# Kernel tuning notes

Hardware: AMD Instinct MI355X
Metric: run time of the kernel (lower is better)

The kernel has to match this reference:

```python
import jax, jax.numpy as jnp
import numpy as np

B, C, H = 2, 256, 64
INTER = 64


def setup_inputs() -> dict:
    key = jax.random.key(0)
    ks = jax.random.split(key, 10)
    scale = 1.0 / np.sqrt(C)
    x = jax.random.normal(ks[0], (B, C, H, H), dtype=jnp.float32)
    # binary hole mask (1 = foreground/hole region)
    mask = jnp.round(jax.random.uniform(ks[1], (B, 1, H, H), dtype=jnp.float32))
    def w(k, shape, s):
        return jax.random.normal(k, shape, dtype=jnp.float32) * s
    return {
        "x": x,
        "mask": mask,
        "w_theta_s": w(ks[2], (INTER, C), scale),
        "w_phi_s": w(ks[3], (INTER, C), scale),
        "w_gate_s": w(ks[4], (INTER, C), scale),
        "w_theta_c": w(ks[5], (INTER, C), scale),
        "w_phi_c": w(ks[6], (INTER, C), scale),
        "w_gate_c": w(ks[7], (INTER, C), scale),
        "w_out": w(ks[8], (C, INTER), 1.0 / np.sqrt(INTER)),
    }


def _nonlocal_branch(q_src, kv_src, w_theta, w_phi, w_gate):
    # q_src, kv_src: [B, C, N]; weights: [inter, C]
    K = jnp.einsum('oc,bcn->bon', w_theta, kv_src)   # [B, inter, N]
    Q = jnp.einsum('oc,bcn->bon', w_phi, q_src)      # [B, inter, N]
    score = jnp.einsum('bom,bon->bmn', Q, K)         # [B, Nq, Nk]
    score = jax.nn.softmax(score, axis=-1)
    V = jnp.einsum('oc,bcn->bon', w_gate, kv_src)    # [B, inter, N]
    feat = jnp.einsum('bon,bmn->bom', V, score)      # [B, inter, Nq]
    return feat, score


def reference(x, mask, w_theta_s, w_phi_s, w_gate_s,
              w_theta_c, w_phi_c, w_gate_c, w_out):
    b, c, h = x.shape[0], x.shape[1], x.shape[2]
    n = h * h
    fg = (x * mask).reshape(b, c, n)          # foreground tokens
    bg = (x * (1.0 - mask)).reshape(b, c, n)  # background tokens
    feat_self, score_self = _nonlocal_branch(fg, fg, w_theta_s, w_phi_s, w_gate_s)
    feat_cross, score_cross = _nonlocal_branch(fg, bg, w_theta_c, w_phi_c, w_gate_c)
    fused = jnp.einsum('co,bon->bcn', w_out, feat_self + feat_cross)
    feat = x + fused.reshape(b, c, h, h)
    return feat, score_self, score_cross
```

## Files before the change

kernel.cpp:

```cpp
#include <hip/hip_runtime.h>
#include <hip/hip_bf16.h>
#include <stdint.h>

#define NBATCH 2
#define NCH    256
#define NTOK   4096
#define NINT   64
#define CHW    64
#define QCOLS  1024
#define NCHQ   (QCOLS/CHW)

typedef float  f32x4  __attribute__((ext_vector_type(4)));
typedef __bf16 bf16x8 __attribute__((ext_vector_type(8)));
union U16x8 { uint4 u; bf16x8 b; };
union PK8   { uint4 u; unsigned short s[8]; };

#define SZBF      ((size_t)NTOK*NINT)
#define RL_OFF_B  ((size_t)4194304)

#define OUT_SELF  ((size_t)2097152)
#define OUT_CROSS ((size_t)35651584)
#define FPART_OFF_F (OUT_SELF)
#define LPART_OFF_F (OUT_SELF + (size_t)4194304)


__device__ inline unsigned short f2bf(float x){
  unsigned int u = __builtin_bit_cast(unsigned int, x);
  u = (u + 0x7FFFu + ((u>>16)&1u)) >> 16;
  return (unsigned short)u;
}
__device__ inline float bf2f(unsigned short s){
  unsigned int u = ((unsigned int)s)<<16;
  return __builtin_bit_cast(float, u);
}

__global__ __launch_bounds__(256) void k_proj(
    const float* __restrict__ x, const float* __restrict__ mask,
    const float* __restrict__ wts, const float* __restrict__ wps,
    const float* __restrict__ wgs, const float* __restrict__ wtc,
    const float* __restrict__ wpc, const float* __restrict__ wgc,
    char* __restrict__ ws)
{
  int nt = blockIdx.x;
  int j  = blockIdx.y;
  int b  = blockIdx.z;
  const float* W; int isBg, mode, arrH, arrL;
  switch (j) {
    case 0: W=wts; isBg=0; mode=2; arrH=2; arrL=3; break;
    case 1: W=wps; isBg=0; mode=0; arrH=0; arrL=1; break;
    case 2: W=wgs; isBg=0; mode=1; arrH=8; arrL=8; break;
    case 3: W=wpc; isBg=0; mode=0; arrH=4; arrL=5; break;
    case 4: W=wtc; isBg=1; mode=2; arrH=6; arrL=7; break;
    default:W=wgc; isBg=1; mode=1; arrH=9; arrL=9; break;
  }
  __shared__ float xm[128*64];
  __shared__ float msk[64];
  int t = threadIdx.x;
  if (t < 64) {
    float m = mask[(size_t)b*NTOK + nt*64 + t];
    msk[t] = isBg ? (1.0f - m) : m;
  }
  __syncthreads();
  const float* xb = x + (size_t)b*NCH*NTOK + nt*64;
  int nl = t & 63;
  int o0 = __builtin_amdgcn_readfirstlane((t>>6)*16);
  const float* Wr = W + (size_t)o0*256;
  float acc[16];
  #pragma unroll
  for (int i=0;i<16;i++) acc[i]=0.0f;
  for (int p=0; p<2; ++p){
    const float* xbp = xb + (size_t)p*128*NTOK;
    for (int it = 0; it < 32; ++it) {
      int flat = it*256 + t; int c = flat>>6, n2 = flat&63;
      xm[flat] = xbp[(size_t)c*NTOK + n2] * msk[n2];
    }
    __syncthreads();
    #pragma unroll 4
    for (int cc=0;cc<128;cc++){
      int c = p*128 + cc;
      float xv = xm[cc*64+nl];
      #pragma unroll
      for (int i=0;i<16;i++) acc[i] += Wr[i*256 + c] * xv;
    }
    __syncthreads();
  }
  int n = nt*64 + nl;
  if (mode==0){
    unsigned short* Ah = (unsigned short*)ws + ((size_t)b*10 + arrH)*SZBF;
    unsigned short* Al = (unsigned short*)ws + ((size_t)b*10 + arrL)*SZBF;
    #pragma unroll
    for (int i=0;i<16;i++){
      float v = acc[i];
      unsigned short h = f2bf(v);
      float r = v - bf2f(h);
      Ah[(size_t)n*NINT + o0+i] = h;
      Al[(size_t)n*NINT + o0+i] = f2bf(r);
    }
  } else if (mode==2){
    unsigned short* Ah = (unsigned short*)ws + ((size_t)b*10 + arrH)*SZBF;
    unsigned short* Al = (unsigned short*)ws + ((size_t)b*10 + arrL)*SZBF;
    int kk  = o0>>5;
    int q40 = (o0>>3)&3;
    size_t base = ((size_t)(n>>4)*2 + kk)*512 + (size_t)(q40*16 + (n&15))*8;
    #pragma unroll
    for (int run=0; run<2; ++run){
      PK8 ph, pl;
      #pragma unroll
      for (int i2=0;i2<8;i2++){
        float v = acc[run*8 + i2];
        unsigned short h = f2bf(v);
        ph.s[i2] = h;
        pl.s[i2] = f2bf(v - bf2f(h));
      }
      *(uint4*)(Ah + base + run*128) = ph.u;
      *(uint4*)(Al + base + run*128) = pl.u;
    }
  } else {
    unsigned short* VF = (unsigned short*)ws + ((size_t)b*10 + arrH)*SZBF;
    size_t cBase = (((size_t)nt*8 + ((nl>>5)&1)*4 + (o0>>4)))*512
                 + (size_t)((nl>>3)&3)*128 + (nl&7);
    #pragma unroll
    for (int i=0;i<16;i++) VF[cBase + (size_t)i*8] = f2bf(acc[i]);
  }
}

__global__ __launch_bounds__(256,2) void k_s1(char* __restrict__ ws, float* __restrict__ out)
{
  __shared__ __align__(16) unsigned short lP[4][1024];

  int blk = blockIdx.x;
  int xcd = blk & 7, idx = blk >> 3;
  int bbr = xcd >> 1;
  int unit = ((xcd & 1) << 6) | idx;
  int qtr = unit & 3, mb2 = unit >> 2;
  int b = bbr >> 1, br = bbr & 1;
  const unsigned short* Qh  = (const unsigned short*)ws + ((size_t)b*10 + (br?4:0))*SZBF;
  const unsigned short* Ql  = Qh + SZBF;
  const unsigned short* KFh = (const unsigned short*)ws + ((size_t)b*10 + (br?6:2))*SZBF;
  const unsigned short* KFl = KFh + SZBF;
  const unsigned short* VF  = (const unsigned short*)ws + ((size_t)b*10 + (br?9:8))*SZBF;

  int t = threadIdx.x, lane = t&63, w = t>>6;
  int rowb = lane&15, q4 = lane>>4, ko = q4*8;
  int mA = mb2*128 + w*16, mB = mA + 64;

  unsigned short* lPw = lP[w];

  U16x8 qhA[2], qlA[2], qhB[2], qlB[2];
  #pragma unroll
  for (int kk=0;kk<2;kk++){
    qhA[kk].u = *(const uint4*)(Qh + (size_t)(mA+rowb)*NINT + kk*32 + ko);
    qlA[kk].u = *(const uint4*)(Ql + (size_t)(mA+rowb)*NINT + kk*32 + ko);
    qhB[kk].u = *(const uint4*)(Qh + (size_t)(mB+rowb)*NINT + kk*32 + ko);
    qlB[kk].u = *(const uint4*)(Ql + (size_t)(mB+rowb)*NINT + kk*32 + ko);
  }

  f32x4 facA[4], facB[4];
  #pragma unroll
  for (int ot=0;ot<4;ot++){ facA[ot]=(f32x4){0,0,0,0}; facB[ot]=(f32x4){0,0,0,0}; }
  float LaccA = 0.0f, LaccB = 0.0f;

  for (int ch=0; ch<NCHQ; ++ch){
    int n0  = qtr*QCOLS + ch*CHW;
    int r16 = n0>>4;
    U16x8 akh[4][2], akl[4][2];
    #pragma unroll
    for (int t8=0; t8<4; ++t8)
      #pragma unroll
      for (int kk=0; kk<2; ++kk){
        size_t cb = ((size_t)(r16 + t8)*2 + kk)*512 + (size_t)lane*8;
        akh[t8][kk].u = *(const uint4*)(KFh + cb);
        akl[t8][kk].u = *(const uint4*)(KFl + cb);
      }
    U16x8 av[2][4];
    #pragma unroll
    for (int kk4=0; kk4<2; ++kk4)
      #pragma unroll
      for (int ot=0; ot<4; ++ot){
        size_t cb = ((size_t)(n0>>6)*8 + kk4*4 + ot)*512 + (size_t)lane*8;
        av[kk4][ot].u = *(const uint4*)(VF + cb);
      }

    #pragma unroll
    for (int hf=0; hf<2; ++hf){
      const U16x8* qh = hf ? qhB : qhA;
      const U16x8* ql = hf ? qlB : qlA;
      f32x4* fac      = hf ? facB : facA;
      float& Lacc     = hf ? LaccB : LaccA;
      #pragma unroll
      for (int t8=0; t8<4; ++t8){
        f32x4 s = {0.0f,0.0f,0.0f,0.0f};
        #pragma unroll
        for (int kk=0; kk<2; ++kk){
          s = __builtin_amdgcn_mfma_f32_16x16x32_bf16(akh[t8][kk].b, qh[kk].b, s, 0,0,0);
          s = __builtin_amdgcn_mfma_f32_16x16x32_bf16(akh[t8][kk].b, ql[kk].b, s, 0,0,0);
          s = __builtin_amdgcn_mfma_f32_16x16x32_bf16(akl[t8][kk].b, qh[kk].b, s, 0,0,0);
        }
        float p0=__expf(s[0]), p1=__expf(s[1]), p2=__expf(s[2]), p3=__expf(s[3]);
        Lacc += (p0+p1)+(p2+p3);
        unsigned int lo = (unsigned int)f2bf(p0) | ((unsigned int)f2bf(p1)<<16);
        unsigned int hi = (unsigned int)f2bf(p2) | ((unsigned int)f2bf(p3)<<16);
        uint2 pk; pk.x = lo; pk.y = hi;
        int g  = t8*2 + (q4>>1);
        int gs = g ^ (rowb&7);
        *(uint2*)(lPw + rowb*64 + gs*8 + (q4&1)*4) = pk;
      }
      #pragma unroll
      for (int kk4=0; kk4<2; ++kk4){
        int rs = (kk4*4 + q4) ^ (rowb&7);
        U16x8 pa;
        pa.u = *(const uint4*)(lPw + rowb*64 + rs*8);
        #pragma unroll
        for (int ot=0; ot<4; ++ot)
          fac[ot] = __builtin_amdgcn_mfma_f32_16x16x32_bf16(pa.b, av[kk4][ot].b, fac[ot], 0,0,0);
      }
    }
  }

  #pragma unroll
  for (int hf=0; hf<2; ++hf){
    int   m0   = hf ? mB : mA;
    float Lacc = hf ? LaccB : LaccA;
    f32x4* fac = hf ? facB : facA;
    #pragma unroll
    for (int d=16; d<64; d<<=1) Lacc += __shfl_xor(Lacc, d, 64);
    if (q4==0)
      out[LPART_OFF_F + (size_t)(bbr*4+qtr)*NTOK + m0 + rowb] = Lacc;
    float* FP = out + FPART_OFF_F + (size_t)(bbr*4+qtr)*NTOK*NINT;
    #pragma unroll
    for (int ot=0; ot<4; ++ot)
      #pragma unroll
      for (int r=0; r<4; ++r)
        FP[(size_t)(m0 + q4*4 + r)*NINT + ot*16 + rowb] = fac[ot][r];
  }
}

__global__ __launch_bounds__(256) void k_epi(
    const float* __restrict__ x, const float* __restrict__ wout,
    char* __restrict__ ws, float* __restrict__ out)
{
  int nt = blockIdx.x, b = blockIdx.y;
  int t = threadIdx.x;
  const float* FP = out + FPART_OFF_F;
  const float* LP = out + LPART_OFF_F;
  float* rL = (float*)(ws + RL_OFF_B);
  __shared__ float fs[32][65];
  __shared__ float rls[2][32];
  int b0 = b*2, b1 = b*2+1;
  if (t < 64){
    int hb = t>>5, rloc = t&31;
    int bb = b*2 + hb;
    int row = nt*32 + rloc;
    float L = 0.0f;
    #pragma unroll
    for (int q=0;q<4;q++) L += LP[(size_t)(bb*4+q)*NTOK + row];
    float r = 1.0f / L;
    rls[hb][rloc] = r;
    rL[(size_t)bb*NTOK + row] = r;
  }
  __syncthreads();
  for (int it=0; it<8; ++it){
    int flat = it*256 + t; int n_l = flat>>6, o = flat&63;
    int row = nt*32 + n_l;
    float s0=0.0f, s1=0.0f;
    #pragma unroll
    for (int q=0;q<4;q++){
      s0 += FP[((size_t)(b0*4+q)*NTOK + row)*NINT + o];
      s1 += FP[((size_t)(b1*4+q)*NTOK + row)*NINT + o];
    }
    fs[n_l][o] = s0*rls[0][n_l] + s1*rls[1][n_l];
  }
  __syncthreads();
  int nl = t&31, cg = t>>5, c0 = cg*32;
  float f[64];
  #pragma unroll
  for (int o=0;o<64;o++) f[o] = fs[nl][o];
  const float* wr = wout + (size_t)c0*64;
  int row = nt*32 + nl;
  for (int cc=0; cc<32; ++cc){
    int c = c0 + cc;
    float acc = x[((size_t)b*NCH + c)*NTOK + row];
    #pragma unroll
    for (int o=0;o<64;o++) acc += wr[cc*64+o]*f[o];
    out[((size_t)b*NCH + c)*NTOK + row] = acc;
  }
}

__global__ __launch_bounds__(256,4) void k_s2(const char* __restrict__ ws, float* __restrict__ out)
{
  int blk = blockIdx.x;
  int xcd = blk & 7, idx = blk >> 3;
  int bbr = xcd >> 1;
  int unit = ((xcd & 1) << 7) | idx;
  int qtr = unit & 3, mb = unit >> 2;
  int b = bbr >> 1, br = bbr & 1;
  const unsigned short* Qh  = (const unsigned short*)ws + ((size_t)b*10 + (br?4:0))*SZBF;
  const unsigned short* Ql  = Qh + SZBF;
  const unsigned short* KFh = (const unsigned short*)ws + ((size_t)b*10 + (br?6:2))*SZBF;
  const unsigned short* KFl = KFh + SZBF;

  int t = threadIdx.x, lane = t&63, w = t>>6;
  int rowb = lane&15, q4 = lane>>4, ko = q4*8;
  int m0 = mb*64 + w*16, mrow = m0 + rowb;

  float rLp = ((const float*)(ws + RL_OFF_B))[(size_t)bbr*NTOK + mrow];

  U16x8 qh[2], ql[2];
  #pragma unroll
  for (int kk=0;kk<2;kk++){
    qh[kk].u = *(const uint4*)(Qh + (size_t)mrow*NINT + kk*32 + ko);
    ql[kk].u = *(const uint4*)(Ql + (size_t)mrow*NINT + kk*32 + ko);
  }

  float* outS = out + (br ? OUT_CROSS : OUT_SELF) + (size_t)b*NTOK*NTOK;

  for (int ch=0; ch<NCHQ; ++ch){
    int n0  = qtr*QCOLS + ch*CHW;
    int r16 = n0>>4;
    #pragma unroll
    for (int t8=0; t8<4; ++t8){
      f32x4 s = {0.0f,0.0f,0.0f,0.0f};
      #pragma unroll
      for (int kk=0; kk<2; ++kk){
        size_t cb = ((size_t)(r16 + t8)*2 + kk)*512 + (size_t)lane*8;
        U16x8 ah, al;
        ah.u = *(const uint4*)(KFh + cb);
        al.u = *(const uint4*)(KFl + cb);
        s = __builtin_amdgcn_mfma_f32_16x16x32_bf16(ah.b, qh[kk].b, s, 0,0,0);
        s = __builtin_amdgcn_mfma_f32_16x16x32_bf16(ah.b, ql[kk].b, s, 0,0,0);
        s = __builtin_amdgcn_mfma_f32_16x16x32_bf16(al.b, qh[kk].b, s, 0,0,0);
      }
      f32x4 p;
      p[0] = __expf(s[0])*rLp; p[1] = __expf(s[1])*rLp;
      p[2] = __expf(s[2])*rLp; p[3] = __expf(s[3])*rLp;
      __builtin_nontemporal_store(p,
          (f32x4*)(outS + (size_t)mrow*NTOK + n0 + t8*16 + q4*4));
    }
  }
}

extern "C" void kernel_launch(void* const* d_in, const int* in_sizes, int n_in,
                              void* d_out, int out_size, void* d_ws, size_t ws_size,
                              hipStream_t stream)
{
  const float* x    = (const float*)d_in[0];
  const float* mask = (const float*)d_in[1];
  const float* wts  = (const float*)d_in[2];
  const float* wps  = (const float*)d_in[3];
  const float* wgs  = (const float*)d_in[4];
  const float* wtc  = (const float*)d_in[5];
  const float* wpc  = (const float*)d_in[6];
  const float* wgc  = (const float*)d_in[7];
  const float* wout = (const float*)d_in[8];
  float* out = (float*)d_out;
  char*  ws  = (char*)d_ws;
  (void)in_sizes; (void)n_in; (void)out_size; (void)ws_size;

  k_proj <<<dim3(64,6,NBATCH), 256, 0, stream>>>(x, mask, wts, wps, wgs, wtc, wpc, wgc, ws);
  k_s1   <<<dim3(512), 256, 0, stream>>>(ws, out);
  k_epi  <<<dim3(128,NBATCH), 256, 0, stream>>>(x, wout, ws, out);
  k_s2   <<<dim3(1024), 256, 0, stream>>>(ws, out);
}
```

Before: 487.0 us.

## Process two query row tiles per wave in k_s2, nontemporal partial stores

k_s2 now computes two 16-row query tiles per wave (128 rows per block), so each key fragment load from global memory feeds twice as many MFMAs. The grid is halved and launch bounds lowered to allow more registers. Separately, k_s1's partial feature and L stores and k_epi's partial loads use nontemporal hints to reduce cache pollution. The trade-off is fewer resident waves and higher register pressure in the store-bound score kernel.

```diff
diff --git a/kernel.cpp b/kernel.cpp
--- a/kernel.cpp
+++ b/kernel.cpp
@@ -225,13 +225,15 @@
     #pragma unroll
     for (int d=16; d<64; d<<=1) Lacc += __shfl_xor(Lacc, d, 64);
     if (q4==0)
-      out[LPART_OFF_F + (size_t)(bbr*4+qtr)*NTOK + m0 + rowb] = Lacc;
+      __builtin_nontemporal_store(Lacc,
+          out + LPART_OFF_F + (size_t)(bbr*4+qtr)*NTOK + m0 + rowb);
     float* FP = out + FPART_OFF_F + (size_t)(bbr*4+qtr)*NTOK*NINT;
     #pragma unroll
     for (int ot=0; ot<4; ++ot)
       #pragma unroll
       for (int r=0; r<4; ++r)
-        FP[(size_t)(m0 + q4*4 + r)*NINT + ot*16 + rowb] = fac[ot][r];
+        __builtin_nontemporal_store(fac[ot][r],
+            FP + (size_t)(m0 + q4*4 + r)*NINT + ot*16 + rowb);
   }
 }
 
@@ -265,8 +267,8 @@
     float s0=0.0f, s1=0.0f;
     #pragma unroll
     for (int q=0;q<4;q++){
-      s0 += FP[((size_t)(b0*4+q)*NTOK + row)*NINT + o];
-      s1 += FP[((size_t)(b1*4+q)*NTOK + row)*NINT + o];
+      s0 += __builtin_nontemporal_load(FP + ((size_t)(b0*4+q)*NTOK + row)*NINT + o);
+      s1 += __builtin_nontemporal_load(FP + ((size_t)(b1*4+q)*NTOK + row)*NINT + o);
     }
     fs[n_l][o] = s0*rls[0][n_l] + s1*rls[1][n_l];
   }
@@ -286,13 +288,13 @@
   }
 }
 
-__global__ __launch_bounds__(256,4) void k_s2(const char* __restrict__ ws, float* __restrict__ out)
+__global__ __launch_bounds__(256,2) void k_s2(const char* __restrict__ ws, float* __restrict__ out)
 {
   int blk = blockIdx.x;
   int xcd = blk & 7, idx = blk >> 3;
   int bbr = xcd >> 1;
-  int unit = ((xcd & 1) << 7) | idx;
-  int qtr = unit & 3, mb = unit >> 2;
+  int unit = ((xcd & 1) << 6) | idx;
+  int qtr = unit & 3, mb2 = unit >> 2;
   int b = bbr >> 1, br = bbr & 1;
   const unsigned short* Qh  = (const unsigned short*)ws + ((size_t)b*10 + (br?4:0))*SZBF;
   const unsigned short* Ql  = Qh + SZBF;
@@ -301,40 +303,55 @@
 
   int t = threadIdx.x, lane = t&63, w = t>>6;
   int rowb = lane&15, q4 = lane>>4, ko = q4*8;
-  int m0 = mb*64 + w*16, mrow = m0 + rowb;
-
-  float rLp = ((const float*)(ws + RL_OFF_B))[(size_t)bbr*NTOK + mrow];
-
-  U16x8 qh[2], ql[2];
+  int mA = mb2*128 + w*16, mB = mA + 64;
+  int mrowA = mA + rowb,   mrowB = mB + rowb;
+
+  const float* rL = (const float*)(ws + RL_OFF_B) + (size_t)bbr*NTOK;
+  float rLpA = rL[mrowA], rLpB = rL[mrowB];
+
+  U16x8 qhA[2], qlA[2], qhB[2], qlB[2];
   #pragma unroll
   for (int kk=0;kk<2;kk++){
-    qh[kk].u = *(const uint4*)(Qh + (size_t)mrow*NINT + kk*32 + ko);
-    ql[kk].u = *(const uint4*)(Ql + (size_t)mrow*NINT + kk*32 + ko);
+    qhA[kk].u = *(const uint4*)(Qh + (size_t)mrowA*NINT + kk*32 + ko);
+    qlA[kk].u = *(const uint4*)(Ql + (size_t)mrowA*NINT + kk*32 + ko);
+    qhB[kk].u = *(const uint4*)(Qh + (size_t)mrowB*NINT + kk*32 + ko);
+    qlB[kk].u = *(const uint4*)(Ql + (size_t)mrowB*NINT + kk*32 + ko);
   }
 
   float* outS = out + (br ? OUT_CROSS : OUT_SELF) + (size_t)b*NTOK*NTOK;
+  float* outA = outS + (size_t)mrowA*NTOK;
+  float* outB = outS + (size_t)mrowB*NTOK;
 
   for (int ch=0; ch<NCHQ; ++ch){
     int n0  = qtr*QCOLS + ch*CHW;
     int r16 = n0>>4;
     #pragma unroll
     for (int t8=0; t8<4; ++t8){
-      f32x4 s = {0.0f,0.0f,0.0f,0.0f};
+      U16x8 ah[2], al[2];
       #pragma unroll
       for (int kk=0; kk<2; ++kk){
         size_t cb = ((size_t)(r16 + t8)*2 + kk)*512 + (size_t)lane*8;
-        U16x8 ah, al;
-        ah.u = *(const uint4*)(KFh + cb);
-        al.u = *(const uint4*)(KFl + cb);
-        s = __builtin_amdgcn_mfma_f32_16x16x32_bf16(ah.b, qh[kk].b, s, 0,0,0);
-        s = __builtin_amdgcn_mfma_f32_16x16x32_bf16(ah.b, ql[kk].b, s, 0,0,0);
-        s = __builtin_amdgcn_mfma_f32_16x16x32_bf16(al.b, qh[kk].b, s, 0,0,0);
-      }
-      f32x4 p;
-      p[0] = __expf(s[0])*rLp; p[1] = __expf(s[1])*rLp;
-      p[2] = __expf(s[2])*rLp; p[3] = __expf(s[3])*rLp;
-      __builtin_nontemporal_store(p,
-          (f32x4*)(outS + (size_t)mrow*NTOK + n0 + t8*16 + q4*4));
+        ah[kk].u = *(const uint4*)(KFh + cb);
+        al[kk].u = *(const uint4*)(KFl + cb);
+      }
+      f32x4 sA = {0.0f,0.0f,0.0f,0.0f}, sB = {0.0f,0.0f,0.0f,0.0f};
+      #pragma unroll
+      for (int kk=0; kk<2; ++kk){
+        sA = __builtin_amdgcn_mfma_f32_16x16x32_bf16(ah[kk].b, qhA[kk].b, sA, 0,0,0);
+        sA = __builtin_amdgcn_mfma_f32_16x16x32_bf16(ah[kk].b, qlA[kk].b, sA, 0,0,0);
+        sA = __builtin_amdgcn_mfma_f32_16x16x32_bf16(al[kk].b, qhA[kk].b, sA, 0,0,0);
+        sB = __builtin_amdgcn_mfma_f32_16x16x32_bf16(ah[kk].b, qhB[kk].b, sB, 0,0,0);
+        sB = __builtin_amdgcn_mfma_f32_16x16x32_bf16(ah[kk].b, qlB[kk].b, sB, 0,0,0);
+        sB = __builtin_amdgcn_mfma_f32_16x16x32_bf16(al[kk].b, qhB[kk].b, sB, 0,0,0);
+      }
+      f32x4 pA, pB;
+      pA[0] = __expf(sA[0])*rLpA; pA[1] = __expf(sA[1])*rLpA;
+      pA[2] = __expf(sA[2])*rLpA; pA[3] = __expf(sA[3])*rLpA;
+      pB[0] = __expf(sB[0])*rLpB; pB[1] = __expf(sB[1])*rLpB;
+      pB[2] = __expf(sB[2])*rLpB; pB[3] = __expf(sB[3])*rLpB;
+      int coff = n0 + t8*16 + q4*4;
+      __builtin_nontemporal_store(pA, (f32x4*)(outA + coff));
+      __builtin_nontemporal_store(pB, (f32x4*)(outB + coff));
     }
   }
 }
@@ -359,5 +376,5 @@
   k_proj <<<dim3(64,6,NBATCH), 256, 0, stream>>>(x, mask, wts, wps, wgs, wtc, wpc, wgc, ws);
   k_s1   <<<dim3(512), 256, 0, stream>>>(ws, out);
   k_epi  <<<dim3(128,NBATCH), 256, 0, stream>>>(x, wout, ws, out);
-  k_s2   <<<dim3(1024), 256, 0, stream>>>(ws, out);
-}
+  k_s2   <<<dim3(512), 256, 0, stream>>>(ws, out);
+}
```

Measured after the change: 509.1 us. 4.5% more time.
